# Kernel tuning notes

Measured on AMD Instinct MI355X. Metric: run time of the kernel, lower is better.

Reference implementation:

```python
import jax, jax.numpy as jnp
import numpy as np

N = 50000
E = 800000
IN_C = 128
HID = 32
HEADS = 4
G = 512      # number of graphs in batch
OUT_C = 100
NEG_SLOPE = 0.2
EPS = 1e-16


def _gat_params(key, f_in, heads, c):
    k1, k2, k3, k4 = jax.random.split(key, 4)
    s = 1.0 / np.sqrt(f_in)
    return {
        'W': jax.random.uniform(k1, (heads * c, f_in), jnp.float32, -s, s),
        'att_src': jax.random.normal(k2, (heads, c), jnp.float32) * 0.1,
        'att_dst': jax.random.normal(k3, (heads, c), jnp.float32) * 0.1,
        'b': jnp.zeros((heads * c,), jnp.float32),
    }


def setup_inputs() -> dict:
    key = jax.random.key(0)
    ks = jax.random.split(key, 8)
    x = jax.random.normal(ks[0], (N, IN_C), jnp.float32)
    edge_index = jax.random.randint(ks[1], (2, E), 0, N, jnp.int64)
    batch = jnp.sort(jax.random.randint(ks[2], (N,), 0, G, jnp.int64))
    p1 = _gat_params(ks[3], IN_C, HEADS, HID)
    p2 = _gat_params(ks[4], HEADS * HID, HEADS, HID)
    p3 = _gat_params(ks[5], HEADS * HID, HEADS, HID)
    s = 1.0 / np.sqrt(HEADS * HID)
    fc_W = jax.random.uniform(ks[6], (OUT_C, HEADS * HID), jnp.float32, -s, s)
    fc_b = jnp.zeros((OUT_C,), jnp.float32)
    return {
        'x': x, 'edge_index': edge_index, 'batch': batch,
        'W1': p1['W'], 'as1': p1['att_src'], 'ad1': p1['att_dst'], 'b1': p1['b'],
        'W2': p2['W'], 'as2': p2['att_src'], 'ad2': p2['att_dst'], 'b2': p2['b'],
        'W3': p3['W'], 'as3': p3['att_src'], 'ad3': p3['att_dst'], 'b3': p3['b'],
        'fc_W': fc_W, 'fc_b': fc_b,
    }


def gat_conv(x, src, dst, W, att_src, att_dst, b):
    # x: [N, F_in] -> h: [N, H, C]
    h = (x @ W.T).reshape(N, HEADS, HID)
    a_src = jnp.einsum('nhc,hc->nh', h, att_src)   # [N, H]
    a_dst = jnp.einsum('nhc,hc->nh', h, att_dst)
    alpha = a_src[src] + a_dst[dst]                 # [E', H]
    alpha = jax.nn.leaky_relu(alpha, NEG_SLOPE)
    # segment softmax over incoming edges of each dst node
    m = jax.ops.segment_max(alpha, dst, num_segments=N)
    alpha = jnp.exp(alpha - m[dst])
    denom = jax.ops.segment_sum(alpha, dst, num_segments=N)
    alpha = alpha / (denom[dst] + EPS)
    msg = alpha[:, :, None] * h[src]                # [E', H, C]
    out = jax.ops.segment_sum(msg, dst, num_segments=N)
    return out.reshape(N, HEADS * HID) + b


def reference(x, edge_index, batch,
              W1, as1, ad1, b1, W2, as2, ad2, b2, W3, as3, ad3, b3,
              fc_W, fc_b):
    # add self loops (PyG GATConv default)
    loops = jnp.arange(N, dtype=edge_index.dtype)
    src = jnp.concatenate([edge_index[0], loops])
    dst = jnp.concatenate([edge_index[1], loops])
    h = jax.nn.elu(gat_conv(x, src, dst, W1, as1, ad1, b1))
    h = jax.nn.elu(gat_conv(h, src, dst, W2, as2, ad2, b2))
    h = jax.nn.elu(gat_conv(h, src, dst, W3, as3, ad3, b3))
    # global mean pool over graphs
    sums = jax.ops.segment_sum(h, batch, num_segments=G)        # [G, H*C]
    cnts = jax.ops.segment_sum(jnp.ones((N,), h.dtype), batch, num_segments=G)
    pooled = sums / jnp.maximum(cnts, 1.0)[:, None]
    # dropout p=0.5 is identity in eval mode
    return pooled @ fc_W.T + fc_b
```

## Files before the change

kernel.cpp:

```cpp
#include <hip/hip_runtime.h>
#include <math.h>

#define NN 50000
#define EE 800000
#define EP (EE + NN)
#define GG 512
#define OUTC 100
#define NEG 0.2f
#define STRIDE 64

typedef __attribute__((ext_vector_type(8))) short bf16x8;
typedef __attribute__((ext_vector_type(8))) short s16x8;
typedef __attribute__((ext_vector_type(8))) unsigned short us8;
typedef __attribute__((ext_vector_type(4))) float f32x4;

__device__ inline ushort f2bf(float v) {
  unsigned u = __float_as_uint(v);
  unsigned r = (u + 0x7fff + ((u >> 16) & 1)) >> 16;
  return (ushort)r;
}

__global__ __launch_bounds__(256) void k_scatter(const int* __restrict__ ei,
    int* __restrict__ cursor, ushort* __restrict__ srcs) {
  int e = blockIdx.x * 256 + threadIdx.x;
  if (e >= EP) return;
  int s, d;
  if (e < EE) { s = ei[e]; d = ei[EE + e]; } else { s = e - EE; d = s; }
  int pos = atomicAdd(&cursor[d], 1);
  if (pos < STRIDE) srcs[(d << 6) + pos] = (ushort)s;
}

__global__ __launch_bounds__(256) void k_prep(
    const float* __restrict__ W0, const float* __restrict__ W1, const float* __restrict__ W2,
    const float* __restrict__ as0, const float* __restrict__ as1, const float* __restrict__ as2,
    const float* __restrict__ ad0, const float* __restrict__ ad1, const float* __restrict__ ad2,
    ushort* __restrict__ hi, ushort* __restrict__ lo) {
  int layer = blockIdx.y;
  const float* W  = (layer == 0) ? W0 : (layer == 1) ? W1 : W2;
  const float* av = (layer == 0) ? as0 : (layer == 1) ? as1 : as2;
  const float* dv = (layer == 0) ? ad0 : (layer == 1) ? ad1 : ad2;
  ushort* hiL = hi + (size_t)layer * 144 * 128;
  ushort* loL = lo + (size_t)layer * 144 * 128;
  int idx = blockIdx.x * 256 + threadIdx.x;
  if (blockIdx.x < 64) {
    float v = W[idx];
    ushort hb = f2bf(v);
    float hf = __uint_as_float(((unsigned)hb) << 16);
    hiL[idx] = hb;
    loL[idx] = f2bf(v - hf);
  } else {
    int j2 = idx - 64 * 256;
    int j = j2 >> 7, k = j2 & 127;
    int head = j & 3;
    const float* vec = (j < 4) ? &av[head * 32] : &dv[head * 32];
    float dot = 0.f;
#pragma unroll
    for (int c = 0; c < 32; c++) dot += W[(head * 32 + c) * 128 + k] * vec[c];
    ushort hb = f2bf(dot);
    float hf = __uint_as_float(((unsigned)hb) << 16);
    hiL[(128 + j) * 128 + k] = hb;
    loL[(128 + j) * 128 + k] = f2bf(dot - hf);
    hiL[(136 + j) * 128 + k] = 0;
    loL[(136 + j) * 128 + k] = 0;
  }
}

__global__ __launch_bounds__(256) void k_gemm_mfma(const float* __restrict__ feat,
    const ushort* __restrict__ Whi, const ushort* __restrict__ Wlo,
    short* __restrict__ hq, float* __restrict__ scalef,
    float* __restrict__ asrcf, float* __restrict__ adstf) {
  __shared__ ushort Ahi[128 * 128];
  __shared__ ushort Alo[128 * 128];
  int n0 = blockIdx.x * 128;
  int t = threadIdx.x;
  {
    int row = t >> 1, half = t & 1;
    int n = n0 + row;
    int sw = row & 15;
    if (n < NN) {
      const float4* src = (const float4*)&feat[(size_t)n * 128 + half * 64];
#pragma unroll
      for (int i = 0; i < 8; i++) {
        float4 a = src[2 * i], b = src[2 * i + 1];
        float vv[8] = {a.x, a.y, a.z, a.w, b.x, b.y, b.z, b.w};
        us8 hh, ll;
#pragma unroll
        for (int j = 0; j < 8; j++) {
          ushort hb = f2bf(vv[j]);
          float hf = __uint_as_float(((unsigned)hb) << 16);
          hh[j] = hb;
          ll[j] = f2bf(vv[j] - hf);
        }
        int pc = (half * 8 + i) ^ sw;
        *(us8*)&Ahi[row * 128 + pc * 8] = hh;
        *(us8*)&Alo[row * 128 + pc * 8] = ll;
      }
    } else {
      us8 z = (us8)0;
#pragma unroll
      for (int i = 0; i < 8; i++) {
        int pc = (half * 8 + i) ^ sw;
        *(us8*)&Ahi[row * 128 + pc * 8] = z;
        *(us8*)&Alo[row * 128 + pc * 8] = z;
      }
    }
  }
  __syncthreads();

  int wave = t >> 6, lane = t & 63;
  int quad = lane >> 4, r16 = lane & 15;
  f32x4 acc[2][8];
#pragma unroll
  for (int mt = 0; mt < 2; mt++)
#pragma unroll
    for (int nt = 0; nt < 8; nt++) acc[mt][nt] = (f32x4)0.f;

  for (int ks = 0; ks < 4; ks++) {
    bf16x8 bh[8], bl[8];
#pragma unroll
    for (int nt = 0; nt < 8; nt++) {
      size_t wo = (size_t)(nt * 16 + r16) * 128 + ks * 32 + quad * 8;
      bh[nt] = *(const bf16x8*)&Whi[wo];
      bl[nt] = *(const bf16x8*)&Wlo[wo];
    }
#pragma unroll
    for (int mt = 0; mt < 2; mt++) {
      int row = wave * 32 + mt * 16 + r16;
      int pc = (ks * 4 + quad) ^ (row & 15);
      bf16x8 ah = *(const bf16x8*)&Ahi[row * 128 + pc * 8];
      bf16x8 al = *(const bf16x8*)&Alo[row * 128 + pc * 8];
#pragma unroll
      for (int nt = 0; nt < 8; nt++) {
        acc[mt][nt] = __builtin_amdgcn_mfma_f32_16x16x32_bf16(ah, bh[nt], acc[mt][nt], 0, 0, 0);
        acc[mt][nt] = __builtin_amdgcn_mfma_f32_16x16x32_bf16(al, bh[nt], acc[mt][nt], 0, 0, 0);
        acc[mt][nt] = __builtin_amdgcn_mfma_f32_16x16x32_bf16(ah, bl[nt], acc[mt][nt], 0, 0, 0);
      }
    }
  }

  f32x4 aug[2];
  aug[0] = (f32x4)0.f; aug[1] = (f32x4)0.f;
  for (int ks = 0; ks < 4; ks++) {
    size_t wo = (size_t)(128 + r16) * 128 + ks * 32 + quad * 8;
    bf16x8 bh = *(const bf16x8*)&Whi[wo];
    bf16x8 bl = *(const bf16x8*)&Wlo[wo];
#pragma unroll
    for (int mt = 0; mt < 2; mt++) {
      int row = wave * 32 + mt * 16 + r16;
      int pc = (ks * 4 + quad) ^ (row & 15);
      bf16x8 ah = *(const bf16x8*)&Ahi[row * 128 + pc * 8];
      bf16x8 al = *(const bf16x8*)&Alo[row * 128 + pc * 8];
      aug[mt] = __builtin_amdgcn_mfma_f32_16x16x32_bf16(ah, bh, aug[mt], 0, 0, 0);
      aug[mt] = __builtin_amdgcn_mfma_f32_16x16x32_bf16(al, bh, aug[mt], 0, 0, 0);
      aug[mt] = __builtin_amdgcn_mfma_f32_16x16x32_bf16(ah, bl, aug[mt], 0, 0, 0);
    }
  }

#pragma unroll
  for (int mt = 0; mt < 2; mt++) {
#pragma unroll
    for (int reg = 0; reg < 4; reg++) {
      float am = 0.f;
#pragma unroll
      for (int nt = 0; nt < 8; nt++) am = fmaxf(am, fabsf(acc[mt][nt][reg]));
#pragma unroll
      for (int off = 1; off < 16; off <<= 1) am = fmaxf(am, __shfl_xor(am, off));
      int node = n0 + wave * 32 + mt * 16 + quad * 4 + reg;
      if (node < NN) {
        float amc = fmaxf(am, 1e-20f);
        float rq = 32767.f / amc;
        if (r16 == 0) scalef[node] = amc * (1.f / 32767.f);
        if (r16 < 4) asrcf[node * 4 + r16] = aug[mt][reg];
        else if (r16 < 8) adstf[node * 4 + r16 - 4] = aug[mt][reg];
        short* dq = &hq[(size_t)node * 128 + r16];
#pragma unroll
        for (int nt = 0; nt < 8; nt++)
          dq[nt * 16] = (short)__float2int_rn(acc[mt][nt][reg] * rq);
      }
    }
  }
}

__global__ __launch_bounds__(256) void k_gather(const short* __restrict__ hq,
    const float* __restrict__ scalef,
    const float4* __restrict__ asrc, const float4* __restrict__ adst,
    const int* __restrict__ cursor, const ushort* __restrict__ srcs,
    const float* __restrict__ bias, float* __restrict__ outf) {
  __shared__ int s_src[4][4][16];
  __shared__ float s_w[4][4][72];
  __shared__ float s_e[4][4][72];

  int wave = threadIdx.x >> 6, lane = threadIdx.x & 63;
  int grp = lane >> 4;
  int gl = lane & 15;
  int node = blockIdx.x * 16 + wave * 4 + grp;

  int deg = 0, e0 = 0;
  float4 ad = make_float4(0.f, 0.f, 0.f, 0.f);
  if (node < NN) {
    deg = min(cursor[node], STRIDE);
    e0 = node << 6;
    ad = adst[node];
  }
  int c0 = gl << 3;
  int head = gl >> 2;

  float acc[8];
#pragma unroll
  for (int i = 0; i < 8; i++) acc[i] = 0.f;
  float wsum = 0.f;

  int rounds = (deg + 15) >> 4;
  for (int r = 0; r < rounds; r++) {
    int base = r << 4;
    int j = base + gl;
    int sn = 0;
    float w0 = 0.f, w1 = 0.f, w2 = 0.f, w3 = 0.f, sc = 0.f;
    if (j < deg) {
      sn = srcs[e0 + j];
      float4 a = asrc[sn];
      sc = scalef[sn];
      float v;
      v = a.x + ad.x; v = v > 0.f ? v : NEG * v; w0 = expf(v);
      v = a.y + ad.y; v = v > 0.f ? v : NEG * v; w1 = expf(v);
      v = a.z + ad.z; v = v > 0.f ? v : NEG * v; w2 = expf(v);
      v = a.w + ad.w; v = v > 0.f ? v : NEG * v; w3 = expf(v);
    }
    s_src[wave][grp][gl] = sn << 7;
    float* wp = &s_w[wave][grp][gl << 2];
    wp[0] = w0 * sc; wp[1] = w1 * sc; wp[2] = w2 * sc; wp[3] = w3 * sc;
    float* ep = &s_e[wave][grp][gl << 2];
    ep[0] = w0; ep[1] = w1; ep[2] = w2; ep[3] = w3;
    __builtin_amdgcn_s_waitcnt(0);

    int cnt = min(16, deg - base);
    int cntp = (cnt + 3) & ~3;
    for (int k = 0; k < cntp; k += 4) {
      int ra = s_src[wave][grp][k + 0];
      int rb = s_src[wave][grp][k + 1];
      int rc = s_src[wave][grp][k + 2];
      int rd = s_src[wave][grp][k + 3];
      float wa = s_w[wave][grp][((k + 0) << 2) | head];
      float wb = s_w[wave][grp][((k + 1) << 2) | head];
      float wc = s_w[wave][grp][((k + 2) << 2) | head];
      float wd = s_w[wave][grp][((k + 3) << 2) | head];
      wsum += s_e[wave][grp][((k + 0) << 2) | head]
            + s_e[wave][grp][((k + 1) << 2) | head]
            + s_e[wave][grp][((k + 2) << 2) | head]
            + s_e[wave][grp][((k + 3) << 2) | head];
      s16x8 qa = *(const s16x8*)&hq[ra + c0];
      s16x8 qb = *(const s16x8*)&hq[rb + c0];
      s16x8 qc = *(const s16x8*)&hq[rc + c0];
      s16x8 qd = *(const s16x8*)&hq[rd + c0];
#pragma unroll
      for (int i = 0; i < 8; i++) acc[i] = fmaf(wa, (float)qa[i], acc[i]);
#pragma unroll
      for (int i = 0; i < 8; i++) acc[i] = fmaf(wb, (float)qb[i], acc[i]);
#pragma unroll
      for (int i = 0; i < 8; i++) acc[i] = fmaf(wc, (float)qc[i], acc[i]);
#pragma unroll
      for (int i = 0; i < 8; i++) acc[i] = fmaf(wd, (float)qd[i], acc[i]);
    }
  }

  if (node < NN) {
    float rcp = 1.f / (wsum + 1e-16f);
    float o[8];
#pragma unroll
    for (int i = 0; i < 8; i++) {
      float v = acc[i] * rcp + bias[c0 + i];
      o[i] = v > 0.f ? v : expm1f(v);
    }
    *(float4*)&outf[(size_t)node * 128 + c0] = make_float4(o[0], o[1], o[2], o[3]);
    *(float4*)&outf[(size_t)node * 128 + c0 + 4] = make_float4(o[4], o[5], o[6], o[7]);
  }
}

__global__ __launch_bounds__(128) void k_pool(const float* __restrict__ feat,
    const int* __restrict__ batch, float* __restrict__ pooled, float* __restrict__ cnt) {
  int n0 = blockIdx.x * 32;
  int c = threadIdx.x;
  float acc = 0.f; int curg = -1;
  for (int i = 0; i < 32; i++) {
    int n = n0 + i;
    if (n >= NN) break;
    int g = batch[n];
    if (g != curg) {
      if (curg >= 0) atomicAdd(&pooled[curg * 128 + c], acc);
      acc = 0.f; curg = g;
    }
    acc += feat[n * 128 + c];
  }
  if (curg >= 0) atomicAdd(&pooled[curg * 128 + c], acc);
  if (threadIdx.x == 0) {
    float cc = 0.f; int cg = -1;
    for (int i = 0; i < 32; i++) {
      int n = n0 + i;
      if (n >= NN) break;
      int g = batch[n];
      if (g != cg) { if (cg >= 0) atomicAdd(&cnt[cg], cc); cc = 0.f; cg = g; }
      cc += 1.f;
    }
    if (cg >= 0) atomicAdd(&cnt[cg], cc);
  }
}

__global__ __launch_bounds__(128) void k_fc(const float* __restrict__ pooled,
    const float* __restrict__ cnt, const float* __restrict__ fcW,
    const float* __restrict__ fcb, float* __restrict__ out) {
  int g = blockIdx.x;
  __shared__ float p[128];
  int t = threadIdx.x;
  float inv = 1.0f / fmaxf(cnt[g], 1.0f);
  p[t] = pooled[g * 128 + t] * inv;
  __syncthreads();
  if (t < OUTC) {
    float acc = fcb[t];
    const float4* wr = (const float4*)&fcW[t * 128];
    const float4* pp = (const float4*)p;
#pragma unroll
    for (int i = 0; i < 32; i++) {
      float4 w = wr[i], pv = pp[i];
      acc = fmaf(w.x, pv.x, fmaf(w.y, pv.y, fmaf(w.z, pv.z, fmaf(w.w, pv.w, acc))));
    }
    out[g * OUTC + t] = acc;
  }
}

extern "C" void kernel_launch(void* const* d_in, const int* in_sizes, int n_in,
                              void* d_out, int out_size, void* d_ws, size_t ws_size,
                              hipStream_t stream) {
  const float* x    = (const float*)d_in[0];
  const int*   ei   = (const int*)d_in[1];
  const int*   batch= (const int*)d_in[2];
  const float* W1   = (const float*)d_in[3];
  const float* as1  = (const float*)d_in[4];
  const float* ad1  = (const float*)d_in[5];
  const float* b1   = (const float*)d_in[6];
  const float* W2   = (const float*)d_in[7];
  const float* as2  = (const float*)d_in[8];
  const float* ad2  = (const float*)d_in[9];
  const float* b2   = (const float*)d_in[10];
  const float* W3   = (const float*)d_in[11];
  const float* as3  = (const float*)d_in[12];
  const float* ad3  = (const float*)d_in[13];
  const float* b3   = (const float*)d_in[14];
  const float* fcW  = (const float*)d_in[15];
  const float* fcb  = (const float*)d_in[16];
  float* out = (float*)d_out;

  char* p = (char*)d_ws;
  auto alloc = [&](size_t bytes) { char* r = p; p += (bytes + 255) & ~(size_t)255; return r; };
  short* hq     = (short*)alloc((size_t)NN * 128 * 2);
  float* scalef = (float*)alloc((size_t)NN * 4);
  float* buf0   = (float*)alloc((size_t)NN * 128 * 4);
  float* asrc   = (float*)alloc((size_t)NN * 4 * 4);
  float* adst   = (float*)alloc((size_t)NN * 4 * 4);
  char*  zbase  = p;
  int*   cursor = (int*)alloc((size_t)NN * 4);
  float* pooled = (float*)alloc((size_t)GG * 128 * 4);
  float* cnt    = (float*)alloc((size_t)GG * 4);
  size_t zlen   = (size_t)(p - zbase);
  ushort* srcs  = (ushort*)alloc((size_t)NN * STRIDE * 2);
  ushort* whi   = (ushort*)alloc((size_t)3 * 144 * 128 * 2);
  ushort* wlo   = (ushort*)alloc((size_t)3 * 144 * 128 * 2);

  hipMemsetAsync(zbase, 0, zlen, stream);

  k_scatter<<<(EP + 255) / 256, 256, 0, stream>>>(ei, cursor, srcs);
  k_prep<<<dim3(68, 3), 256, 0, stream>>>(W1, W2, W3, as1, as2, as3, ad1, ad2, ad3, whi, wlo);

  const float* bs[3] = {b1, b2, b3};
  const float* fin = x;
  for (int l = 0; l < 3; l++) {
    k_gemm_mfma<<<(NN + 127) / 128, 256, 0, stream>>>(fin,
        whi + (size_t)l * 144 * 128, wlo + (size_t)l * 144 * 128,
        hq, scalef, asrc, adst);
    k_gather<<<(NN + 15) / 16, 256, 0, stream>>>(hq, scalef,
        (const float4*)asrc, (const float4*)adst,
        cursor, srcs, bs[l], buf0);
    fin = buf0;
  }
  k_pool<<<(NN + 31) / 32, 128, 0, stream>>>(buf0, batch, pooled, cnt);
  k_fc<<<GG, 128, 0, stream>>>(pooled, cnt, fcW, fcb, out);
}
```

Before: 385.3 us.

## Partition edge scatter by destination range and handle self-loops inline in gather

```diff
diff --git a/kernel.cpp b/kernel.cpp
--- a/kernel.cpp
+++ b/kernel.cpp
@@ -3,11 +3,13 @@
 
 #define NN 50000
 #define EE 800000
-#define EP (EE + NN)
 #define GG 512
 #define OUTC 100
 #define NEG 0.2f
 #define STRIDE 64
+#define NPART 8
+#define PRNG (NN / NPART)
+#define PCHUNK 4096
 
 typedef __attribute__((ext_vector_type(8))) short bf16x8;
 typedef __attribute__((ext_vector_type(8))) short s16x8;
@@ -22,12 +24,19 @@
 
 __global__ __launch_bounds__(256) void k_scatter(const int* __restrict__ ei,
     int* __restrict__ cursor, ushort* __restrict__ srcs) {
-  int e = blockIdx.x * 256 + threadIdx.x;
-  if (e >= EP) return;
-  int s, d;
-  if (e < EE) { s = ei[e]; d = ei[EE + e]; } else { s = e - EE; d = s; }
-  int pos = atomicAdd(&cursor[d], 1);
-  if (pos < STRIDE) srcs[(d << 6) + pos] = (ushort)s;
+  int part = blockIdx.x & (NPART - 1);
+  int chunk = blockIdx.x >> 3;
+  int lo = part * PRNG, hi = lo + PRNG;
+  int base = chunk * PCHUNK;
+  for (int i = threadIdx.x; i < PCHUNK; i += 256) {
+    int e = base + i;
+    if (e >= EE) break;
+    int d = ei[EE + e];
+    if (d < lo || d >= hi) continue;
+    int s = ei[e];
+    int pos = atomicAdd(&cursor[d], 1);
+    if (pos < STRIDE) srcs[(d << 6) + pos] = (ushort)s;
+  }
 }
 
 __global__ __launch_bounds__(256) void k_prep(
@@ -210,6 +219,22 @@
   for (int i = 0; i < 8; i++) acc[i] = 0.f;
   float wsum = 0.f;
 
+  if (node < NN) {
+    float4 a = asrc[node];
+    float sc = scalef[node];
+    float v, w0, w1, w2, w3;
+    v = a.x + ad.x; v = v > 0.f ? v : NEG * v; w0 = expf(v);
+    v = a.y + ad.y; v = v > 0.f ? v : NEG * v; w1 = expf(v);
+    v = a.z + ad.z; v = v > 0.f ? v : NEG * v; w2 = expf(v);
+    v = a.w + ad.w; v = v > 0.f ? v : NEG * v; w3 = expf(v);
+    float wh = (head == 0) ? w0 : (head == 1) ? w1 : (head == 2) ? w2 : w3;
+    wsum = wh;
+    float ws = wh * sc;
+    s16x8 qs = *(const s16x8*)&hq[(node << 7) + c0];
+#pragma unroll
+    for (int i = 0; i < 8; i++) acc[i] = ws * (float)qs[i];
+  }
+
   int rounds = (deg + 15) >> 4;
   for (int r = 0; r < rounds; r++) {
     int base = r << 4;
@@ -367,7 +392,8 @@
 
   hipMemsetAsync(zbase, 0, zlen, stream);
 
-  k_scatter<<<(EP + 255) / 256, 256, 0, stream>>>(ei, cursor, srcs);
+  int nchunks = (EE + PCHUNK - 1) / PCHUNK;
+  k_scatter<<<NPART * nchunks, 256, 0, stream>>>(ei, cursor, srcs);
   k_prep<<<dim3(68, 3), 256, 0, stream>>>(W1, W2, W3, as1, as2, as3, ad1, ad2, ad3, whi, wlo);
 
   const float* bs[3] = {b1, b2, b3};
```

Result: faster. 372.7 us (-3.3%).
